# Performance work log

Hardware: AMD Instinct MI355X
Metric: run time of the kernel (lower is better)

The kernel has to match this reference:

```python
import jax, jax.numpy as jnp
import numpy as np
import math

B, L, I, H = 32, 2048, 64, 512
HALF = H // 2
DT = 0.05
RHO = 0.99
INPUT_SCALING = 1.0
STD = 1.0
GAMMA_MIN, GAMMA_MAX = 0.5, 1.0
EPS_MIN, EPS_MAX = 0.5, 1.0


def setup_inputs() -> dict:
    key = jax.random.key(0)
    ks = jax.random.split(key, 7)
    x = jax.random.normal(ks[0], (B, L, I), dtype=jnp.float32)
    x2h = jax.random.uniform(ks[1], (I, H), dtype=jnp.float32) * INPUT_SCALING
    h2h = 2.0 * (2.0 * jax.random.uniform(ks[2], (H, H), dtype=jnp.float32) - 1.0)
    # spectral_norm_scaling: rescale so largest singular value == rho
    h2h = h2h * (RHO / jnp.linalg.norm(h2h, ord=2))
    bias = (2.0 * jax.random.uniform(ks[3], (H,), dtype=jnp.float32) - 1.0) * INPUT_SCALING
    gamma = jax.random.uniform(ks[4], (H,), dtype=jnp.float32) * (GAMMA_MAX - GAMMA_MIN) + GAMMA_MIN
    epsilon = jax.random.uniform(ks[5], (H,), dtype=jnp.float32) * (EPS_MAX - EPS_MIN) + EPS_MIN
    # RandomFourierFeature: W_sin = W_cos, shape [half_dim, in_dim]
    W_rff = jax.random.normal(ks[6], (HALF, H), dtype=jnp.float32) * STD
    return {"x": x, "x2h": x2h, "h2h": h2h, "bias": bias,
            "gamma": gamma, "epsilon": epsilon, "W_rff": W_rff}


def _run(x, x2h, h2h, bias, gamma, epsilon, W_rff):
    b = x.shape[0]
    inv_sqrt_half = 1.0 / math.sqrt(HALF)

    def step(carry, xt):
        hy, hz, zsum = carry
        pre = jnp.tanh(xt @ x2h + hy @ h2h + bias)          # [B,H]
        hz = hz + DT * (pre - gamma * hy - epsilon * hz)
        hy = hy + DT * hz
        wx = hy @ W_rff.T                                   # [B,HALF]
        z = jnp.concatenate([jnp.cos(wx), jnp.sin(wx)], axis=-1) * inv_sqrt_half
        return (hy, hz, zsum + z), None

    hy0 = jnp.zeros((b, H), dtype=x.dtype)
    hz0 = jnp.zeros((b, H), dtype=x.dtype)
    zsum0 = jnp.zeros((b, H), dtype=x.dtype)
    (hy, hz, zsum), _ = jax.lax.scan(step, (hy0, hz0, zsum0), jnp.swapaxes(x, 0, 1))
    mu = zsum / x.shape[1]  # mean over time of per-step RFF states
    return mu, hy


def reference(x, x2h, h2h, bias, gamma, epsilon, W_rff):
    return _run(x, x2h, h2h, bias, gamma, epsilon, W_rff)
```

## Files before the change

kernel.cpp:

```cpp
#include <hip/hip_runtime.h>
#include <math.h>

#define Bz 32
#define Lz 2048
#define Iz 64
#define Hz 512
#define HALFz 256
#define DTz 0.05f
#define NMEM 8
#define TPB 512

typedef unsigned long long u64;

__device__ __forceinline__ bool tagok(u64 v, unsigned tag) {
  u64 want = (u64)tag | ((u64)tag << 48);
  return ((v ^ want) & 0xFFFF00000000FFFFull) == 0ull;
}
__device__ __forceinline__ u64 packv(float f, unsigned tag) {
  return (u64)tag | ((u64)__float_as_uint(f) << 16) | ((u64)tag << 48);
}
__device__ __forceinline__ float unpackv(u64 v) {
  return __uint_as_float((unsigned)(v >> 16));
}

__global__ __launch_bounds__(TPB, 2) void coesn_x2(
    const float* __restrict__ x, const float* __restrict__ x2h,
    const float* __restrict__ h2h, const float* __restrict__ bias,
    const float* __restrict__ gam, const float* __restrict__ eps,
    const float* __restrict__ W_rff, u64* __restrict__ Xb,
    u64* __restrict__ Yb, float* __restrict__ out) {
  __shared__ __align__(16) float hyf[2][Hz];
  __shared__ __align__(16) float xb[2][Iz];

  const int b  = blockIdx.x & 31;
  const int m  = blockIdx.x >> 5;
  const int u  = threadIdx.x;
  const int w  = u >> 6;
  const int l  = u & 63;
  const int c0 = m * 64;
  const int j  = ((l & 1) << 2) | (l & 2) | ((l >> 2) & 1);
  const int mycol = c0 + w * 8 + j;
  const int rloc = u >> 4, kseg = u & 15;

  float wreg[8][8];
  {
    const float* hrow = h2h + (size_t)(8 * l) * Hz + c0 + 8 * w;
    #pragma unroll
    for (int r = 0; r < 8; ++r) {
      float4 v0 = *(const float4*)(hrow + (size_t)r * Hz);
      float4 v1 = *(const float4*)(hrow + (size_t)r * Hz + 4);
      wreg[r][0] = v0.x; wreg[r][1] = v0.y; wreg[r][2] = v0.z; wreg[r][3] = v0.w;
      wreg[r][4] = v1.x; wreg[r][5] = v1.y; wreg[r][6] = v1.z; wreg[r][7] = v1.w;
    }
  }
  float xreg[8];
  {
    float4 v0 = *(const float4*)(x2h + (size_t)l * Hz + c0 + 8 * w);
    float4 v1 = *(const float4*)(x2h + (size_t)l * Hz + c0 + 8 * w + 4);
    xreg[0] = v0.x; xreg[1] = v0.y; xreg[2] = v0.z; xreg[3] = v0.w;
    xreg[4] = v1.x; xreg[5] = v1.y; xreg[6] = v1.z; xreg[7] = v1.w;
  }
  float wr[32];
  {
    const float* wp = W_rff + (size_t)(m * 32 + rloc) * Hz + kseg * 32;
    #pragma unroll
    for (int i = 0; i < 32; ++i) wr[i] = wp[i];
  }

  const float bu = bias[mycol];
  const float gu = gam[mycol];
  const float eu = eps[mycol];
  float hy = 0.f, hz = 0.f, zc = 0.f, zs = 0.f;
  hyf[0][u] = 0.f;
  if (u < 16) ((float4*)xb[0])[u] = ((const float4*)(x + (size_t)b * Lz * Iz))[u];
  __syncthreads();

  auto rff_acc = [&](const float* hsrc) {
    float acc = 0.f;
    const float4* hp = (const float4*)hsrc;
    #pragma unroll
    for (int i = 0; i < 8; ++i) {
      int q = kseg * 8 + i;
      float4 h4 = hp[q ^ ((q >> 3) & 7)];
      acc = fmaf(h4.x, wr[4 * i], acc);
      acc = fmaf(h4.y, wr[4 * i + 1], acc);
      acc = fmaf(h4.z, wr[4 * i + 2], acc);
      acc = fmaf(h4.w, wr[4 * i + 3], acc);
    }
    acc += __shfl_xor(acc, 1); acc += __shfl_xor(acc, 2);
    acc += __shfl_xor(acc, 4); acc += __shfl_xor(acc, 8);
    float sv, cv;
    __sincosf(acc, &sv, &cv);
    zc += cv; zs += sv;
  };

  for (int t = 0; t < Lz; ++t) {
    const int cur = t & 1, nxt = cur ^ 1;

    if (u < 16 && t + 1 < Lz)
      ((float4*)xb[nxt])[u] =
          ((const float4*)(x + ((size_t)b * Lz + (t + 1)) * Iz))[u];

    float hv[8];
    {
      const float4* hp = (const float4*)hyf[cur];
      int q0 = 2 * l, q1 = 2 * l + 1;
      float4 h0 = hp[q0 ^ ((q0 >> 3) & 7)];
      float4 h1 = hp[q1 ^ ((q1 >> 3) & 7)];
      hv[0] = h0.x; hv[1] = h0.y; hv[2] = h0.z; hv[3] = h0.w;
      hv[4] = h1.x; hv[5] = h1.y; hv[6] = h1.z; hv[7] = h1.w;
    }
    float a[8] = {0.f, 0.f, 0.f, 0.f, 0.f, 0.f, 0.f, 0.f};
    #pragma unroll
    for (int r = 0; r < 8; ++r) {
      float h = hv[r];
      #pragma unroll
      for (int c = 0; c < 8; ++c) a[c] = fmaf(h, wreg[r][c], a[c]);
    }
    {
      float xv = xb[cur][l];
      #pragma unroll
      for (int c = 0; c < 8; ++c) a[c] = fmaf(xv, xreg[c], a[c]);
    }
    #pragma unroll
    for (int i = 0; i < 4; ++i) {
      float snd = (l & 1) ? a[i] : a[i + 4];
      float rcv = __shfl_xor(snd, 1);
      a[i] = ((l & 1) ? a[i + 4] : a[i]) + rcv;
    }
    #pragma unroll
    for (int i = 0; i < 2; ++i) {
      float snd = (l & 2) ? a[i] : a[i + 2];
      float rcv = __shfl_xor(snd, 2);
      a[i] = ((l & 2) ? a[i + 2] : a[i]) + rcv;
    }
    float s;
    {
      float snd = (l & 4) ? a[0] : a[1];
      float rcv = __shfl_xor(snd, 4);
      s = ((l & 4) ? a[1] : a[0]) + rcv;
    }
    s += __shfl_xor(s, 8); s += __shfl_xor(s, 16); s += __shfl_xor(s, 32);

    s += bu;
    float e2 = __expf(s + s);
    float pre = 1.f - 2.f * __builtin_amdgcn_rcpf(e2 + 1.f);
    float hzn = fmaf(DTz, pre - gu * hy - eu * hz, hz);
    hy = fmaf(DTz, hzn, hy);
    hz = hzn;

    const unsigned tag = (unsigned)(t + 1);
    u64* XA = Xb + ((size_t)nxt * Bz + b) * Hz;
    u64* YA = Yb + ((size_t)nxt * Bz + b) * Hz;

    if (l < 8) {
      u64 pv = packv(hy, tag);
      *(volatile u64*)(XA + mycol) = pv;
      __hip_atomic_store(YA + mycol, pv, __ATOMIC_RELAXED,
                         __HIP_MEMORY_SCOPE_AGENT);
      int q = mycol >> 2;
      hyf[nxt][(q ^ ((q >> 3) & 7)) * 4 + (mycol & 3)] = hy;
    }

    if (t > 0) rff_acc(hyf[cur]);

    if (w != m) {
      u64 v; int it = 0;
      for (;;) {
        v = *(volatile const u64*)(XA + u);
        if (tagok(v, tag)) break;
        if (it >= 2) {
          v = __hip_atomic_load(YA + u, __ATOMIC_RELAXED,
                                __HIP_MEMORY_SCOPE_AGENT);
          if (tagok(v, tag)) break;
        }
        if (++it > (1 << 20)) break;
      }
      int q = u >> 2;
      hyf[nxt][(q ^ ((q >> 3) & 7)) * 4 + (u & 3)] = unpackv(v);
    }
    __syncthreads();
  }

  rff_acc(hyf[0]);

  if (l < 8) out[(size_t)Bz * Hz + (size_t)b * Hz + mycol] = hy;
  if (kseg == 0) {
    const float sc = 0.0625f / 2048.f;
    out[(size_t)b * Hz + m * 32 + rloc] = zc * sc;
    out[(size_t)b * Hz + HALFz + m * 32 + rloc] = zs * sc;
  }
}

#define FMA4(P, S, W) do { (P).x = fmaf((S), (W).x, (P).x); (P).y = fmaf((S), (W).y, (P).y); \
                           (P).z = fmaf((S), (W).z, (P).z); (P).w = fmaf((S), (W).w, (P).w); } while(0)

__global__ __launch_bounds__(512) void coesn_scan_fb(
    const float* __restrict__ x, const float* __restrict__ x2h,
    const float* __restrict__ h2h, const float* __restrict__ bias,
    const float* __restrict__ gam, const float* __restrict__ eps,
    const float* __restrict__ W_rff, float* __restrict__ out) {
  const int b = blockIdx.x;
  const int u = threadIdx.x;
  __shared__ __align__(16) float hy_lds[Hz];
  __shared__ __align__(16) float x_lds[Iz];
  __shared__ float4 part[4][128];
  __shared__ float wx_lds[HALFz];

  float hy = 0.f, hz = 0.f, zsum = 0.f;
  const float bu = bias[u];
  const float gu = gam[u];
  const float eu = eps[u];

  const int kq = u >> 7;
  const int g  = u & 127;
  const int jj = u >> 2;
  const int ks = u & 3;

  const float4* __restrict__ H4 = (const float4*)h2h;
  const float4* __restrict__ X2 = (const float4*)x2h;
  const float4* __restrict__ W4 = (const float4*)W_rff;
  const float4* __restrict__ XG = (const float4*)x;
  const float4* hy4 = (const float4*)hy_lds;

  hy_lds[u] = 0.f;
  if (u < 16) ((float4*)x_lds)[u] = XG[(long)b * Lz * 16 + u];
  __syncthreads();

  for (int t = 0; t < Lz; ++t) {
    float4 p = make_float4(0.f, 0.f, 0.f, 0.f);
    {
      const float4* hp = (const float4*)&hy_lds[kq << 7];
      #pragma unroll 8
      for (int k4 = 0; k4 < 32; ++k4) {
        float4 hv = hp[k4];
        const float4* wr2 = &H4[(size_t)((kq << 7) + (k4 << 2)) * 128 + g];
        float4 w0 = wr2[0]; float4 w1 = wr2[128]; float4 w2 = wr2[256]; float4 w3 = wr2[384];
        FMA4(p, hv.x, w0); FMA4(p, hv.y, w1); FMA4(p, hv.z, w2); FMA4(p, hv.w, w3);
      }
      const float4* xp = (const float4*)&x_lds[kq << 4];
      #pragma unroll
      for (int k4 = 0; k4 < 4; ++k4) {
        float4 xv = xp[k4];
        const float4* wr2 = &X2[(size_t)((kq << 4) + (k4 << 2)) * 128 + g];
        float4 w0 = wr2[0]; float4 w1 = wr2[128]; float4 w2 = wr2[256]; float4 w3 = wr2[384];
        FMA4(p, xv.x, w0); FMA4(p, xv.y, w1); FMA4(p, xv.z, w2); FMA4(p, xv.w, w3);
      }
    }
    part[kq][g] = p;
    __syncthreads();
    {
      const float* pp = (const float*)part;
      float s = (pp[u] + pp[512 + u]) + (pp[1024 + u] + pp[1536 + u]);
      float pre = tanhf(s + bu);
      float hzn = fmaf(DTz, pre - gu * hy - eu * hz, hz);
      hy = fmaf(DTz, hzn, hy);
      hz = hzn;
      hy_lds[u] = hy;
      if (u < 16 && t + 1 < Lz)
        ((float4*)x_lds)[u] = XG[((long)b * Lz + (t + 1)) * 16 + u];
    }
    __syncthreads();
    {
      float4 acc0 = make_float4(0.f,0.f,0.f,0.f), acc1 = make_float4(0.f,0.f,0.f,0.f);
      #pragma unroll 4
      for (int it = 0; it < 32; ++it) {
        int k4 = (it << 2) + ks;
        float4 hv = hy4[k4];
        float4 w0 = W4[(size_t)jj * 128 + k4];
        float4 w1 = W4[(size_t)(jj + 128) * 128 + k4];
        acc0.x = fmaf(hv.x, w0.x, acc0.x); acc0.y = fmaf(hv.y, w0.y, acc0.y);
        acc0.z = fmaf(hv.z, w0.z, acc0.z); acc0.w = fmaf(hv.w, w0.w, acc0.w);
        acc1.x = fmaf(hv.x, w1.x, acc1.x); acc1.y = fmaf(hv.y, w1.y, acc1.y);
        acc1.z = fmaf(hv.z, w1.z, acc1.z); acc1.w = fmaf(hv.w, w1.w, acc1.w);
      }
      float a0 = (acc0.x + acc0.y) + (acc0.z + acc0.w);
      float a1 = (acc1.x + acc1.y) + (acc1.z + acc1.w);
      a0 += __shfl_xor(a0, 1); a0 += __shfl_xor(a0, 2);
      a1 += __shfl_xor(a1, 1); a1 += __shfl_xor(a1, 2);
      if (ks == 0) { wx_lds[jj] = a0; wx_lds[jj + 128] = a1; }
    }
    __syncthreads();
    {
      float v = wx_lds[u & 255];
      zsum += (u < HALFz) ? cosf(v) : sinf(v);
    }
  }
  out[(long)b * Hz + u] = zsum * (0.0625f / 2048.f);
  out[(long)Bz * Hz + (long)b * Hz + u] = hy;
}

extern "C" void kernel_launch(void* const* d_in, const int* in_sizes, int n_in,
                              void* d_out, int out_size, void* d_ws, size_t ws_size,
                              hipStream_t stream) {
  const float* x    = (const float*)d_in[0];
  const float* x2h  = (const float*)d_in[1];
  const float* h2h  = (const float*)d_in[2];
  const float* bias = (const float*)d_in[3];
  const float* gam  = (const float*)d_in[4];
  const float* eps  = (const float*)d_in[5];
  const float* wrff = (const float*)d_in[6];
  float* out = (float*)d_out;

  const size_t NEX = (size_t)2 * Bz * Hz;
  const size_t WS_NEED = 2 * NEX * sizeof(u64);
  if (ws_size >= WS_NEED) {
    u64* Xb = (u64*)d_ws;
    u64* Yb = Xb + NEX;
    hipMemsetAsync(d_ws, 0, WS_NEED, stream);
    void* args[] = { (void*)&x, (void*)&x2h, (void*)&h2h, (void*)&bias,
                     (void*)&gam, (void*)&eps, (void*)&wrff,
                     (void*)&Xb, (void*)&Yb, (void*)&out };
    hipError_t e = hipLaunchCooperativeKernel((const void*)coesn_x2,
                                              dim3(Bz * NMEM), dim3(TPB),
                                              args, 0, stream);
    if (e == hipSuccess) return;
  }
  coesn_scan_fb<<<Bz, 512, 0, stream>>>(x, x2h, h2h, bias, gam, eps, wrff, out);
}
```

Measured before the change: 3.412 ms.

## Overlap cross-block hidden-state exchange with recurrent matvec in a rotated order

Reorders the h2h row ownership so each thread handles one hidden row per peer block, rotated by block index. Each step starts with its own block's local slice, then consumes each peer's slice as it arrives, folding the poll for remote values into the matvec. This replaces the old wait-then-compute step with partial overlap. The tag wait moves to the start of the next step, which lets the RFF accumulation and other work run before polling. It adds a final-step gather after the loop and changes the per-step dependency ordering, which could spin longer if peers are skewed.

```diff
diff --git a/kernel.cpp b/kernel.cpp
--- a/kernel.cpp
+++ b/kernel.cpp
@@ -23,7 +23,7 @@
   return __uint_as_float((unsigned)(v >> 16));
 }
 
-__global__ __launch_bounds__(TPB, 2) void coesn_x2(
+__global__ __launch_bounds__(TPB, 2) void coesn_p8(
     const float* __restrict__ x, const float* __restrict__ x2h,
     const float* __restrict__ h2h, const float* __restrict__ bias,
     const float* __restrict__ gam, const float* __restrict__ eps,
@@ -43,15 +43,13 @@
   const int rloc = u >> 4, kseg = u & 15;
 
   float wreg[8][8];
-  {
-    const float* hrow = h2h + (size_t)(8 * l) * Hz + c0 + 8 * w;
-    #pragma unroll
-    for (int r = 0; r < 8; ++r) {
-      float4 v0 = *(const float4*)(hrow + (size_t)r * Hz);
-      float4 v1 = *(const float4*)(hrow + (size_t)r * Hz + 4);
-      wreg[r][0] = v0.x; wreg[r][1] = v0.y; wreg[r][2] = v0.z; wreg[r][3] = v0.w;
-      wreg[r][4] = v1.x; wreg[r][5] = v1.y; wreg[r][6] = v1.z; wreg[r][7] = v1.w;
-    }
+  #pragma unroll
+  for (int d = 0; d < 8; ++d) {
+    const float* hrow = h2h + (size_t)((((m + d) & 7) << 6) | l) * Hz + c0 + 8 * w;
+    float4 v0 = *(const float4*)(hrow);
+    float4 v1 = *(const float4*)(hrow + 4);
+    wreg[d][0] = v0.x; wreg[d][1] = v0.y; wreg[d][2] = v0.z; wreg[d][3] = v0.w;
+    wreg[d][4] = v1.x; wreg[d][5] = v1.y; wreg[d][6] = v1.z; wreg[d][7] = v1.w;
   }
   float xreg[8];
   {
@@ -96,32 +94,55 @@
 
   for (int t = 0; t < Lz; ++t) {
     const int cur = t & 1, nxt = cur ^ 1;
+    const unsigned tagc = (unsigned)t;
+    u64* XC = Xb + ((size_t)cur * Bz + b) * Hz;
+    u64* YC = Yb + ((size_t)cur * Bz + b) * Hz;
+
+    u64 vv[7];
+    #pragma unroll
+    for (int d = 1; d < 8; ++d)
+      vv[d - 1] = *(volatile const u64*)(XC + ((((m + d) & 7) << 6) | l));
 
     if (u < 16 && t + 1 < Lz)
       ((float4*)xb[nxt])[u] =
           ((const float4*)(x + ((size_t)b * Lz + (t + 1)) * Iz))[u];
 
-    float hv[8];
-    {
-      const float4* hp = (const float4*)hyf[cur];
-      int q0 = 2 * l, q1 = 2 * l + 1;
-      float4 h0 = hp[q0 ^ ((q0 >> 3) & 7)];
-      float4 h1 = hp[q1 ^ ((q1 >> 3) & 7)];
-      hv[0] = h0.x; hv[1] = h0.y; hv[2] = h0.z; hv[3] = h0.w;
-      hv[4] = h1.x; hv[5] = h1.y; hv[6] = h1.z; hv[7] = h1.w;
-    }
     float a[8] = {0.f, 0.f, 0.f, 0.f, 0.f, 0.f, 0.f, 0.f};
-    #pragma unroll
-    for (int r = 0; r < 8; ++r) {
-      float h = hv[r];
+    {
+      int col = c0 + l;
+      int q = col >> 2;
+      float h = hyf[cur][((q ^ ((q >> 3) & 7)) << 2) | (l & 3)];
       #pragma unroll
-      for (int c = 0; c < 8; ++c) a[c] = fmaf(h, wreg[r][c], a[c]);
-    }
-    {
+      for (int c = 0; c < 8; ++c) a[c] = fmaf(h, wreg[0][c], a[c]);
       float xv = xb[cur][l];
       #pragma unroll
       for (int c = 0; c < 8; ++c) a[c] = fmaf(xv, xreg[c], a[c]);
     }
+
+    #pragma unroll
+    for (int d = 1; d < 8; ++d) {
+      const int col = (((m + d) & 7) << 6) | l;
+      u64 v = vv[d - 1];
+      if (!tagok(v, tagc)) {
+        int it = 0;
+        for (;;) {
+          v = *(volatile const u64*)(XC + col);
+          if (tagok(v, tagc)) break;
+          if (it >= 2) {
+            v = __hip_atomic_load(YC + col, __ATOMIC_RELAXED,
+                                  __HIP_MEMORY_SCOPE_AGENT);
+            if (tagok(v, tagc)) break;
+          }
+          if (++it > (1 << 20)) break;
+        }
+      }
+      float h = unpackv(v);
+      int q = col >> 2;
+      hyf[cur][((q ^ ((q >> 3) & 7)) << 2) | (l & 3)] = h;
+      #pragma unroll
+      for (int c = 0; c < 8; ++c) a[c] = fmaf(h, wreg[d][c], a[c]);
+    }
+
     #pragma unroll
     for (int i = 0; i < 4; ++i) {
       float snd = (l & 1) ? a[i] : a[i + 4];
@@ -149,40 +170,47 @@
     hy = fmaf(DTz, hzn, hy);
     hz = hzn;
 
-    const unsigned tag = (unsigned)(t + 1);
-    u64* XA = Xb + ((size_t)nxt * Bz + b) * Hz;
-    u64* YA = Yb + ((size_t)nxt * Bz + b) * Hz;
-
-    if (l < 8) {
-      u64 pv = packv(hy, tag);
-      *(volatile u64*)(XA + mycol) = pv;
-      __hip_atomic_store(YA + mycol, pv, __ATOMIC_RELAXED,
-                         __HIP_MEMORY_SCOPE_AGENT);
-      int q = mycol >> 2;
-      hyf[nxt][(q ^ ((q >> 3) & 7)) * 4 + (mycol & 3)] = hy;
+    {
+      u64* XN = Xb + ((size_t)nxt * Bz + b) * Hz;
+      u64* YN = Yb + ((size_t)nxt * Bz + b) * Hz;
+      if (l < 8) {
+        u64 pv = packv(hy, (unsigned)(t + 1));
+        *(volatile u64*)(XN + mycol) = pv;
+        __hip_atomic_store(YN + mycol, pv, __ATOMIC_RELAXED,
+                           __HIP_MEMORY_SCOPE_AGENT);
+        int q = mycol >> 2;
+        hyf[nxt][((q ^ ((q >> 3) & 7)) << 2) | (mycol & 3)] = hy;
+      }
     }
 
     if (t > 0) rff_acc(hyf[cur]);
 
-    if (w != m) {
+    __syncthreads();
+  }
+
+  {
+    u64* XC = Xb + (size_t)b * Hz;
+    u64* YC = Yb + (size_t)b * Hz;
+    const unsigned tagf = (unsigned)Lz;
+    #pragma unroll
+    for (int d = 1; d < 8; ++d) {
+      const int col = (((m + d) & 7) << 6) | l;
       u64 v; int it = 0;
       for (;;) {
-        v = *(volatile const u64*)(XA + u);
-        if (tagok(v, tag)) break;
+        v = *(volatile const u64*)(XC + col);
+        if (tagok(v, tagf)) break;
         if (it >= 2) {
-          v = __hip_atomic_load(YA + u, __ATOMIC_RELAXED,
+          v = __hip_atomic_load(YC + col, __ATOMIC_RELAXED,
                                 __HIP_MEMORY_SCOPE_AGENT);
-          if (tagok(v, tag)) break;
+          if (tagok(v, tagf)) break;
         }
         if (++it > (1 << 20)) break;
       }
-      int q = u >> 2;
-      hyf[nxt][(q ^ ((q >> 3) & 7)) * 4 + (u & 3)] = unpackv(v);
-    }
-    __syncthreads();
-  }
-
-  rff_acc(hyf[0]);
+      int q = col >> 2;
+      hyf[0][((q ^ ((q >> 3) & 7)) << 2) | (l & 3)] = unpackv(v);
+    }
+    rff_acc(hyf[0]);
+  }
 
   if (l < 8) out[(size_t)Bz * Hz + (size_t)b * Hz + mycol] = hy;
   if (kseg == 0) {
@@ -311,7 +339,7 @@
     void* args[] = { (void*)&x, (void*)&x2h, (void*)&h2h, (void*)&bias,
                      (void*)&gam, (void*)&eps, (void*)&wrff,
                      (void*)&Xb, (void*)&Yb, (void*)&out };
-    hipError_t e = hipLaunchCooperativeKernel((const void*)coesn_x2,
+    hipError_t e = hipLaunchCooperativeKernel((const void*)coesn_p8,
                                               dim3(Bz * NMEM), dim3(TPB),
                                               args, 0, stream);
     if (e == hipSuccess) return;
```

Measured after the change: 5.119 ms. +50.0%, slower.
